# Kernel tuning notes

Hardware: AMD Instinct MI355X
Metric: run time of the kernel (lower is better)

## Reference

```python
import jax, jax.numpy as jnp
import numpy as np

N_VERBS = 500
N_ROLES = 190
VOCAB = 2000
R = 6            # max_role_count
EMB = 512        # embed_hidden == lstm_hidden
MLP = 1024       # mlp_hidden
C = 512          # conv base size
H = W = 7
NP = H * W
NC = C + 2       # conv channels + 2 coord channels


def _lin(k, fan_in, fan_out):
    kw, kb = jax.random.split(k)
    s = 1.0 / np.sqrt(fan_in)
    return (jax.random.uniform(kw, (fan_in, fan_out), jnp.float32, -s, s),
            jax.random.uniform(kb, (fan_out,), jnp.float32, -s, s))


def setup_inputs() -> dict:
    key = jax.random.key(0)
    ks = jax.random.split(key, 16)
    inp = {}
    inp['conv_feat'] = jax.random.normal(ks[0], (2, C, H, W), jnp.float32)
    inp['verbs'] = jax.random.randint(ks[1], (2,), 0, N_VERBS, jnp.int32)
    inp['roles'] = jax.random.randint(ks[2], (2, R), 0, N_ROLES, jnp.int32)
    inp['verb_emb'] = jax.random.normal(ks[3], (N_VERBS, EMB), jnp.float32)
    inp['role_emb'] = jax.random.normal(ks[4], (N_ROLES + 1, EMB), jnp.float32)
    inp['vW1'], inp['vb1'] = _lin(ks[5], NP * C, MLP)
    inp['vW2'], inp['vb2'] = _lin(ks[6], MLP, MLP)
    inp['vW3'], inp['vb3'] = _lin(ks[7], MLP, N_VERBS)
    inp['gW1'], inp['gb1'] = _lin(ks[8], 2 * NC + EMB, MLP)
    inp['gW2'], inp['gb2'] = _lin(ks[9], MLP, MLP)
    inp['gW3'], inp['gb3'] = _lin(ks[10], MLP, 2 * MLP)
    inp['gW4'], inp['gb4'] = _lin(ks[11], 2 * MLP, 4 * MLP)
    inp['fW1'], inp['fb1'] = _lin(ks[12], 4 * MLP, 4 * MLP)
    inp['fW2'], inp['fb2'] = _lin(ks[13], 4 * MLP, 2 * MLP)
    inp['fW3'], inp['fb3'] = _lin(ks[14], 2 * MLP, VOCAB)
    return inp


def _coords():
    c = jnp.linspace(-4.0, 4.0, H)
    x = jnp.broadcast_to(c[None, :], (H, W))   # x varies along width
    y = jnp.broadcast_to(c[:, None], (H, W))   # y varies along height
    return jnp.stack([x, y]).reshape(2, NP).T  # [NP, 2]


def reference(conv_feat, verbs, roles, verb_emb, role_emb,
              vW1, vb1, vW2, vb2, vW3, vb3,
              gW1, gb1, gW2, gb2, gW3, gb3, gW4, gb4,
              fW1, fb1, fW2, fb2, fW3, fb3):
    relu = jax.nn.relu
    B = conv_feat.shape[0]

    # verb head
    flat = conv_feat.reshape(B, NP * C)
    v = relu(flat @ vW1 + vb1)
    v = relu(v @ vW2 + vb2)
    verb_pred = v @ vW3 + vb3                                  # [B, N_VERBS]

    # role-verb query
    rv = (verb_emb[verbs][:, None, :] * role_emb[roles]).reshape(B * R, EMB)

    # per-role conv features + coord channels -> [Bu, NP, NC]
    feat = jnp.broadcast_to(conv_feat[:, None], (B, R, C, H, W)).reshape(B * R, C, NP)
    feat = jnp.concatenate([feat.transpose(0, 2, 1),
                            jnp.broadcast_to(_coords()[None], (B * R, NP, 2))], axis=2)

    # first g layer: concat([o_j, o_i, qst]) @ gW1 == split matmuls + broadcast add
    Wa, Wb, Wc = gW1[:NC], gW1[NC:2 * NC], gW1[2 * NC:]
    A = feat @ Wa          # pairs with conv1 (index j)
    Bm = feat @ Wb         # pairs with conv2 (index i)
    Q = rv @ Wc
    h = relu(A[:, None, :, :] + Bm[:, :, None, :] + Q[:, None, None, :] + gb1)  # [Bu, NP, NP, MLP]
    h = relu(h @ gW2 + gb2)
    h = relu(h @ gW3 + gb3)
    h = relu(h @ gW4 + gb4)                                    # [Bu, NP, NP, 4*MLP]
    g = h.sum(axis=(1, 2))                                     # [Bu, 4*MLP]

    f = relu(g @ fW1 + fb1)
    f = relu(f @ fW2 + fb2)
    f = f @ fW3 + fb3                                          # [Bu, VOCAB]
    role_predict = f.reshape(B, R, VOCAB)
    return verb_pred, role_predict
```

## Files before the change

### kernel.cpp

```cpp
#include <hip/hip_runtime.h>
#include <cstdint>

typedef _Float16 f16;
typedef f16 f16x8 __attribute__((ext_vector_type(8)));
typedef f16 f16x4 __attribute__((ext_vector_type(4)));
typedef float f32x4 __attribute__((ext_vector_type(4)));

#define GROUP_ROWS 2560
#define VALID_ROWS 2401
#define TPG 10
#define NGROUP 12

template <bool B> struct BoolC { static constexpr bool value = B; };

__device__ __forceinline__ void gll16(const void* g, void* l) {
  __builtin_amdgcn_global_load_lds((const __attribute__((address_space(1))) void*)g,
                                   (__attribute__((address_space(3))) void*)l, 16, 0, 0);
}

__global__ void wtrans_all(const float* __restrict__ gW2, const float* __restrict__ gW3,
                           const float* __restrict__ gW4, f16* __restrict__ W2t,
                           f16* __restrict__ W3t, f16* __restrict__ W4t) {
  __shared__ float t[32][33];
  int blk = blockIdx.x;
  const float* W; f16* Wt; int K, N, local;
  if (blk < 1024)      { W = gW2; Wt = W2t; K = 1024; N = 1024; local = blk; }
  else if (blk < 3072) { W = gW3; Wt = W3t; K = 1024; N = 2048; local = blk - 1024; }
  else                 { W = gW4; Wt = W4t; K = 2048; N = 4096; local = blk - 3072; }
  int ntn = N >> 5;
  int k0 = (local / ntn) * 32, n0 = (local % ntn) * 32;
  int tx = threadIdx.x & 31, ty = threadIdx.x >> 5;
#pragma unroll
  for (int j = 0; j < 4; ++j)
    t[ty + j * 8][tx] = W[(size_t)(k0 + ty + j * 8) * N + n0 + tx];
  __syncthreads();
#pragma unroll
  for (int j = 0; j < 4; ++j)
    Wt[(size_t)(n0 + ty + j * 8) * K + k0 + tx] = (f16)t[tx][ty + j * 8];
}

__global__ void build_rv(const float* __restrict__ verb_emb, const float* __restrict__ role_emb,
                         const int* __restrict__ verbs, const int* __restrict__ roles,
                         float* __restrict__ rv) {
  int g = blockIdx.x;
  int b = g / 6;
  int v = verbs[b], ro = roles[g];
  for (int e = threadIdx.x; e < 512; e += 256)
    rv[g * 512 + e] = verb_emb[(size_t)v * 512 + e] * role_emb[(size_t)ro * 512 + e];
}

__global__ void build_AB_part(const float* __restrict__ conv, const float* __restrict__ gW1,
                              float* __restrict__ part) {
  int blk = blockIdx.x;
  int nq = blk & 3, bp = blk >> 2;
  int p = bp % 49, b = bp / 49;
  int n = nq * 256 + threadIdx.x;
  int ky = blockIdx.y;
  int k0 = ky * 66, k1 = k0 + 66;
  if (k1 > 514) k1 = 514;
  float accA = 0.f, accB = 0.f;
  for (int k = k0; k < k1; ++k) {
    float s;
    if (k < 512) s = conv[((size_t)b * 512 + k) * 49 + p];
    else {
      int c7 = (k == 512) ? (p % 7) : (p / 7);
      s = (float)(c7 - 3) * (4.0f / 3.0f);
    }
    accA = fmaf(s, gW1[(size_t)k * 1024 + n], accA);
    accB = fmaf(s, gW1[(size_t)(514 + k) * 1024 + n], accB);
  }
  size_t base = ((size_t)ky * 98 + bp) * 2048;
  part[base + n] = accA;
  part[base + 1024 + n] = accB;
}

__global__ void build_AB_fin(const float* __restrict__ part, float* __restrict__ A,
                             float* __restrict__ Bm) {
  int idx = blockIdx.x * 256 + threadIdx.x;
  if (idx >= 98 * 2048) return;
  int bp = idx >> 11, rem = idx & 2047;
  float s = 0.f;
#pragma unroll
  for (int ky = 0; ky < 8; ++ky) s += part[((size_t)ky * 98 + bp) * 2048 + rem];
  if (rem < 1024) A[(size_t)bp * 1024 + rem] = s;
  else Bm[(size_t)bp * 1024 + (rem - 1024)] = s;
}

__global__ void build_h1(const float* __restrict__ A, const float* __restrict__ Bm,
                         const float* __restrict__ Q, const float* __restrict__ gb1,
                         f16* __restrict__ h1, int g0) {
  int rc = blockIdx.x;
  int gl = rc / GROUP_ROWS;
  int li = rc % GROUP_ROWS;
  int g = g0 + gl;
  int b = g / 6;
  int kk = threadIdx.x * 4;
  f16x4* dst = (f16x4*)(h1 + (size_t)rc * 1024 + kk);
  if (li >= VALID_ROWS) {
    f16x4 z = {(f16)0.f, (f16)0.f, (f16)0.f, (f16)0.f};
    *dst = z;
    return;
  }
  int i = li / 49, j = li % 49;
  const float4 a = *(const float4*)(A + ((size_t)b * 49 + j) * 1024 + kk);
  const float4 bb = *(const float4*)(Bm + ((size_t)b * 49 + i) * 1024 + kk);
  const float4 q = *(const float4*)(Q + (size_t)g * 1024 + kk);
  const float4 bi = *(const float4*)(gb1 + kk);
  float v0 = a.x + bb.x + q.x + bi.x;
  float v1 = a.y + bb.y + q.y + bi.y;
  float v2 = a.z + bb.z + q.z + bi.z;
  float v3 = a.w + bb.w + q.w + bi.w;
  f16x4 r;
  r.x = (f16)(v0 > 0.f ? v0 : 0.f);
  r.y = (f16)(v1 > 0.f ? v1 : 0.f);
  r.z = (f16)(v2 > 0.f ? v2 : 0.f);
  r.w = (f16)(v3 > 0.f ? v3 : 0.f);
  *dst = r;
}

#define WV4 asm volatile("s_waitcnt vmcnt(4)" ::: "memory")
#define WV0 asm volatile("s_waitcnt vmcnt(0)" ::: "memory")

#define LDSA(buf, mf, cc) (*(const f16x8*)(ldsc + (buf)*32768 + arow + (mf)*2048 + (cc)*16))
#define LDSB(buf, nf, cc) (*(const f16x8*)(ldsc + 65536 + (buf)*32768 + brow + (nf)*2048 + (cc)*16))

#define LOADB(BF, buf) { \
  BF[0][0] = LDSB(buf, 0, c0); BF[0][1] = LDSB(buf, 0, c1); \
  BF[1][0] = LDSB(buf, 1, c0); BF[1][1] = LDSB(buf, 1, c1); \
  BF[2][0] = LDSB(buf, 2, c0); BF[2][1] = LDSB(buf, 2, c1); \
  BF[3][0] = LDSB(buf, 3, c0); BF[3][1] = LDSB(buf, 3, c1); }

#define STAGE_A(t, h) { \
  const f16* _g = Aglo + (long)(h) * (128L * K) + (long)(t) * 64; \
  char* _l = ldsc + ((t)&1)*32768 + ((h)*128 + wave*16)*128; \
  gll16(_g, _l); gll16(_g + 8L*K, _l + 1024); }

#define STAGE_B(t, h) { \
  const f16* _g = Bglo + (long)(h) * (128L * K) + (long)(t) * 64; \
  char* _l = ldsc + 65536 + ((t)&1)*32768 + ((h)*128 + wave*16)*128; \
  gll16(_g, _l); gll16(_g + 8L*K, _l + 1024); }

#define PHASE(q, buf, BF, STG, WT, POST) { \
  f16x8 a00 = LDSA(buf, 2*(q), c0);   f16x8 a01 = LDSA(buf, 2*(q), c1); \
  f16x8 a10 = LDSA(buf, 2*(q)+1, c0); f16x8 a11 = LDSA(buf, 2*(q)+1, c1); \
  STG; \
  WT; \
  __builtin_amdgcn_s_barrier(); \
  __builtin_amdgcn_s_setprio(1); \
  _Pragma("unroll") \
  for (int nf = 0; nf < 4; ++nf) { \
    acc[2*(q)][nf]   = __builtin_amdgcn_mfma_f32_16x16x32_f16(a00, BF[nf][0], acc[2*(q)][nf], 0, 0, 0); \
    acc[2*(q)][nf]   = __builtin_amdgcn_mfma_f32_16x16x32_f16(a01, BF[nf][1], acc[2*(q)][nf], 0, 0, 0); \
    acc[2*(q)+1][nf] = __builtin_amdgcn_mfma_f32_16x16x32_f16(a10, BF[nf][0], acc[2*(q)+1][nf], 0, 0, 0); \
    acc[2*(q)+1][nf] = __builtin_amdgcn_mfma_f32_16x16x32_f16(a11, BF[nf][1], acc[2*(q)+1][nf], 0, 0, 0); \
  } \
  __builtin_amdgcn_s_setprio(0); \
  POST; \
  __builtin_amdgcn_s_barrier(); \
}

template <int FUSED>
__global__ __launch_bounds__(512, 2)
void gemm256(const f16* __restrict__ A, const f16* __restrict__ Bt,
             const float* __restrict__ bias, f16* __restrict__ C,
             float* __restrict__ P, int N, int K, int ntiles, int mtile_off) {
  __shared__ __align__(16) char ldsbuf[131072];
  char* ldsc = ldsbuf;
  const int tid = threadIdx.x;
  const int wave = tid >> 6, lane = tid & 63;
  const int wm = wave >> 2, wn = wave & 3;
  const int lr = lane & 15, lk = lane >> 4;
  const int c0 = lk ^ (lr & 7), c1 = c0 ^ 4;
  const int arow = (wm * 128 + lr) * 128;
  const int brow = (wn * 64 + lr) * 128;

  int nwg = gridDim.x, id = blockIdx.x;
  int qq = nwg >> 3, rr8 = nwg & 7;
  int xcd = id & 7, idx = id >> 3;
  int wg = (xcd < rr8 ? xcd * (qq + 1) : rr8 * (qq + 1) + (xcd - rr8) * qq) + idx;
  const int mtile = wg / ntiles, ntile = wg % ntiles;
  const long m0 = (long)mtile * 256, n0 = (long)ntile * 256;

  const int srow = lane >> 3;
  const int schunk = (lane & 7) ^ srow;
  const f16* Aglo = A + (m0 + wave * 16 + srow) * (long)K + schunk * 8;
  const f16* Bglo = Bt + (n0 + wave * 16 + srow) * (long)K + schunk * 8;

  f32x4 acc[8][4] = {};
  f16x8 bFa[4][2], bFb[4][2];

  const int NI = K >> 7;

  STAGE_B(0, 0); STAGE_B(0, 1);
  STAGE_A(0, 0); STAGE_A(0, 1);
  STAGE_B(1, 0); STAGE_B(1, 1);
  WV4;
  __builtin_amdgcn_s_barrier();
  LOADB(bFa, 0);

  auto run_iter = [&](int i, auto lastTag) {
    constexpr bool LAST = decltype(lastTag)::value;
    PHASE(0, 0, bFa, STAGE_A(2*i+1, 0), ;, ;);
    PHASE(1, 0, bFa, STAGE_A(2*i+1, 1), ;, ;);
    PHASE(2, 0, bFa, if constexpr (!LAST) STAGE_B(2*i+2, 0), ;, ;);
    PHASE(3, 0, bFa, if constexpr (!LAST) STAGE_B(2*i+2, 1),
                 if constexpr (LAST) { WV0; } else { WV4; },
                 LOADB(bFb, 1));
    PHASE(0, 1, bFb, if constexpr (!LAST) STAGE_A(2*i+2, 0), ;, ;);
    PHASE(1, 1, bFb, if constexpr (!LAST) STAGE_A(2*i+2, 1), ;, ;);
    PHASE(2, 1, bFb, if constexpr (!LAST) STAGE_B(2*i+3, 0), ;, ;);
    PHASE(3, 1, bFb, if constexpr (!LAST) STAGE_B(2*i+3, 1),
                 if constexpr (!LAST) { WV4; },
                 if constexpr (!LAST) LOADB(bFa, 0));
  };
#pragma unroll 1
  for (int i = 0; i < NI - 1; ++i) run_iter(i, BoolC<false>{});
  run_iter(NI - 1, BoolC<true>{});

  if (FUSED == 0) {
    __syncthreads();
    f16* lt = (f16*)ldsc;
#pragma unroll
    for (int mf = 0; mf < 8; ++mf) {
#pragma unroll
      for (int nf = 0; nf < 4; ++nf) {
        const int col = wn * 64 + nf * 16 + lr;
        const float bv = bias[n0 + col];
#pragma unroll
        for (int r = 0; r < 4; ++r) {
          const int row = wm * 128 + mf * 16 + lk * 4 + r;
          float v = acc[mf][nf][r] + bv;
          v = v > 0.f ? v : 0.f;
          lt[row * 256 + (col ^ (((row >> 2) & 3) << 4))] = (f16)v;
        }
      }
    }
    __syncthreads();
    const int r0 = tid >> 5, ch = tid & 31;
#pragma unroll
    for (int p = 0; p < 16; ++p) {
      const int row = p * 16 + r0;
      const int chs = ch ^ (((row >> 2) & 3) << 1);
      f16x8 v = *(const f16x8*)(lt + row * 256 + chs * 8);
      *(f16x8*)(C + (m0 + row) * N + n0 + ch * 8) = v;
    }
  } else {
    float* csum = (float*)ldsc;
    const int mrel = (mtile % TPG) * 256 + wm * 128;
#pragma unroll
    for (int nf = 0; nf < 4; ++nf) {
      const int col = (int)n0 + wn * 64 + nf * 16 + lr;
      const float bv = bias[col];
      float s = 0.f;
#pragma unroll
      for (int mf = 0; mf < 8; ++mf) {
        const int rb = mrel + mf * 16 + lk * 4;
#pragma unroll
        for (int r = 0; r < 4; ++r) {
          float v = acc[mf][nf][r] + bv;
          v = v > 0.f ? v : 0.f;
          if (rb + r < VALID_ROWS) s += v;
        }
      }
      s += __shfl_xor(s, 16);
      s += __shfl_xor(s, 32);
      if (lk == 0) csum[wm * 256 + wn * 64 + nf * 16 + lr] = s;
    }
    __syncthreads();
    for (int t = tid; t < 256; t += 512)
      P[(long)(mtile_off + mtile) * N + n0 + t] = csum[t] + csum[256 + t];
  }
}

__global__ void reduce_g(const float* __restrict__ P, float* __restrict__ g) {
  int idx = blockIdx.x * 256 + threadIdx.x;
  if (idx >= NGROUP * 4096) return;
  int gi = idx >> 12, n = idx & 4095;
  float s = 0.f;
#pragma unroll
  for (int t = 0; t < TPG; ++t) s += P[(size_t)(gi * TPG + t) * 4096 + n];
  g[idx] = s;
}

template <int M>
__global__ void skinny_part(const float* __restrict__ X, const float* __restrict__ W,
                            float* __restrict__ P, int K, int N, int kchunk) {
  int n = blockIdx.x * 256 + threadIdx.x;
  int k0 = blockIdx.y * kchunk;
  int k1 = k0 + kchunk;
  if (k1 > K) k1 = K;
  if (n >= N) return;
  float acc[M];
#pragma unroll
  for (int m = 0; m < M; ++m) acc[m] = 0.f;
#pragma unroll 4
  for (int k = k0; k < k1; ++k) {
    float w = W[(size_t)k * N + n];
#pragma unroll
    for (int m = 0; m < M; ++m) acc[m] = fmaf(X[(size_t)m * K + k], w, acc[m]);
  }
#pragma unroll
  for (int m = 0; m < M; ++m) P[((size_t)blockIdx.y * M + m) * N + n] = acc[m];
}

template <int RELU>
__global__ void skinny_fin(const float* __restrict__ P, const float* __restrict__ bias,
                           float* __restrict__ dst, int M, int N, int KC) {
  int idx = blockIdx.x * 256 + threadIdx.x;
  if (idx >= M * N) return;
  int m = idx / N, n = idx - m * N;
  float s = bias ? bias[n] : 0.f;
  for (int kc = 0; kc < KC; ++kc) s += P[((size_t)kc * M + m) * N + n];
  if (RELU) s = s > 0.f ? s : 0.f;
  dst[idx] = s;
}

static inline void skinny(const float* X, const float* W, const float* bias, float* dst,
                          float* sp, int Mrows, int K, int N, int relu, hipStream_t stream) {
  int nx = (N + 255) / 256;
  int KC = 1024 / nx;
  if (KC > 256) KC = 256;
  int kmax = K / 16;
  if (kmax < 1) kmax = 1;
  if (KC > kmax) KC = kmax;
  int kchunk = (K + KC - 1) / KC;
  dim3 g1(nx, KC);
  if (Mrows == 2)
    skinny_part<2><<<g1, 256, 0, stream>>>(X, W, sp, K, N, kchunk);
  else
    skinny_part<12><<<g1, 256, 0, stream>>>(X, W, sp, K, N, kchunk);
  int blocks = (Mrows * N + 255) / 256;
  if (relu)
    skinny_fin<1><<<blocks, 256, 0, stream>>>(sp, bias, dst, Mrows, N, KC);
  else
    skinny_fin<0><<<blocks, 256, 0, stream>>>(sp, bias, dst, Mrows, N, KC);
}

extern "C" void kernel_launch(void* const* d_in, const int* in_sizes, int n_in,
                              void* d_out, int out_size, void* d_ws, size_t ws_size,
                              hipStream_t stream) {
  const float* conv = (const float*)d_in[0];
  const int* verbs = (const int*)d_in[1];
  const int* roles = (const int*)d_in[2];
  const float* verb_emb = (const float*)d_in[3];
  const float* role_emb = (const float*)d_in[4];
  const float* vW1 = (const float*)d_in[5];
  const float* vb1 = (const float*)d_in[6];
  const float* vW2 = (const float*)d_in[7];
  const float* vb2 = (const float*)d_in[8];
  const float* vW3 = (const float*)d_in[9];
  const float* vb3 = (const float*)d_in[10];
  const float* gW1 = (const float*)d_in[11];
  const float* gb1 = (const float*)d_in[12];
  const float* gW2 = (const float*)d_in[13];
  const float* gb2 = (const float*)d_in[14];
  const float* gW3 = (const float*)d_in[15];
  const float* gb3 = (const float*)d_in[16];
  const float* gW4 = (const float*)d_in[17];
  const float* gb4 = (const float*)d_in[18];
  const float* fW1 = (const float*)d_in[19];
  const float* fb1 = (const float*)d_in[20];
  const float* fW2 = (const float*)d_in[21];
  const float* fb2 = (const float*)d_in[22];
  const float* fW3 = (const float*)d_in[23];
  const float* fb3 = (const float*)d_in[24];
  float* out = (float*)d_out;

  char* w = (char*)d_ws;
  auto alloc = [&](size_t bytes) {
    char* p = w;
    w += (bytes + 255) & ~(size_t)255;
    return p;
  };
  f16* W2t = (f16*)alloc((size_t)1024 * 1024 * 2);
  f16* W3t = (f16*)alloc((size_t)2048 * 1024 * 2);
  f16* W4t = (f16*)alloc((size_t)4096 * 2048 * 2);
  float* P4 = (float*)alloc((size_t)NGROUP * TPG * 4096 * 4);
  float* Abuf = (float*)alloc((size_t)2 * 49 * 1024 * 4);
  float* Bbuf = (float*)alloc((size_t)2 * 49 * 1024 * 4);
  float* Qbuf = (float*)alloc((size_t)12 * 1024 * 4);
  float* rvb = (float*)alloc((size_t)12 * 512 * 4);
  float* gbuf = (float*)alloc((size_t)12 * 4096 * 4);
  float* sp = (float*)alloc((size_t)64 * 12 * 4096 * 4);
  float* f1b = (float*)alloc((size_t)12 * 4096 * 4);
  float* f2b = (float*)alloc((size_t)12 * 2048 * 4);
  float* v1b = (float*)alloc((size_t)2 * 1024 * 4);
  float* v2b = (float*)alloc((size_t)2 * 1024 * 4);

  size_t used = (size_t)(w - (char*)d_ws);
  size_t remain = ws_size > used ? ws_size - used : 0;
  static const int opts[6] = {12, 6, 4, 3, 2, 1};
  int gpc = 1;
  for (int i = 0; i < 6; ++i) {
    size_t need = (size_t)opts[i] * GROUP_ROWS * 4096 * 2 + 4096;
    if (need <= remain) { gpc = opts[i]; break; }
  }
  f16* h1 = (f16*)alloc((size_t)gpc * GROUP_ROWS * 1024 * 2);
  f16* h2 = (f16*)alloc((size_t)gpc * GROUP_ROWS * 1024 * 2);
  f16* h3 = (f16*)alloc((size_t)gpc * GROUP_ROWS * 2048 * 2);
  int nchunks = NGROUP / gpc;

  wtrans_all<<<1024 + 2048 + 8192, 256, 0, stream>>>(gW2, gW3, gW4, W2t, W3t, W4t);

  build_rv<<<12, 256, 0, stream>>>(verb_emb, role_emb, verbs, roles, rvb);
  build_AB_part<<<dim3(98 * 4, 8), 256, 0, stream>>>(conv, gW1, sp);
  build_AB_fin<<<(98 * 2048 + 255) / 256, 256, 0, stream>>>(sp, Abuf, Bbuf);
  skinny(rvb, gW1 + (size_t)1028 * 1024, nullptr, Qbuf, sp, 12, 512, 1024, 0, stream);

  skinny(conv, vW1, vb1, v1b, sp, 2, 25088, 1024, 1, stream);
  skinny(v1b, vW2, vb2, v2b, sp, 2, 1024, 1024, 1, stream);
  skinny(v2b, vW3, vb3, out, sp, 2, 1024, 500, 0, stream);

  for (int c = 0; c < nchunks; ++c) {
    int g0 = c * gpc;
    int Mc = gpc * GROUP_ROWS;
    int mt = Mc / 256;
    build_h1<<<Mc, 256, 0, stream>>>(Abuf, Bbuf, Qbuf, gb1, h1, g0);
    gemm256<0><<<4 * mt, 512, 0, stream>>>(h1, W2t, gb2, h2, nullptr, 1024, 1024, 4, 0);
    gemm256<0><<<8 * mt, 512, 0, stream>>>(h2, W3t, gb3, h3, nullptr, 2048, 1024, 8, 0);
    gemm256<1><<<16 * mt, 512, 0, stream>>>(h3, W4t, gb4, nullptr, P4, 4096, 2048, 16, g0 * TPG);
  }
  reduce_g<<<(NGROUP * 4096 + 255) / 256, 256, 0, stream>>>(P4, gbuf);

  skinny(gbuf, fW1, fb1, f1b, sp, 12, 4096, 4096, 1, stream);
  skinny(f1b, fW2, fb2, f2b, sp, 12, 4096, 2048, 1, stream);
  skinny(f2b, fW3, fb3, out + 1000, sp, 12, 2048, 2000, 0, stream);

  (void)in_sizes; (void)n_in; (void)out_size; (void)ws_size;
}
```

Before: 934.5 us.

## Fuse h1 construction into first g-layer GEMM A-operand staging

Removes the separate build_h1 kernel and its f16 h1 buffer. The first GEMM (FUSED==2) now builds each A tile on the fly from A, Bm, Q and gb1 with fp32 loads, add, relu and an f16 convert, writing straight to LDS. This saves the h1 write and re-read and one launch. In exchange, the staging goes from async global_load_lds to synchronous register loads plus VALU work inside the MFMA pipeline, which needs extra lgkmcnt waits and may stall the main loop.

```diff
diff --git a/kernel.cpp b/kernel.cpp
--- a/kernel.cpp
+++ b/kernel.cpp
@@ -86,40 +86,9 @@
   else Bm[(size_t)bp * 1024 + (rem - 1024)] = s;
 }
 
-__global__ void build_h1(const float* __restrict__ A, const float* __restrict__ Bm,
-                         const float* __restrict__ Q, const float* __restrict__ gb1,
-                         f16* __restrict__ h1, int g0) {
-  int rc = blockIdx.x;
-  int gl = rc / GROUP_ROWS;
-  int li = rc % GROUP_ROWS;
-  int g = g0 + gl;
-  int b = g / 6;
-  int kk = threadIdx.x * 4;
-  f16x4* dst = (f16x4*)(h1 + (size_t)rc * 1024 + kk);
-  if (li >= VALID_ROWS) {
-    f16x4 z = {(f16)0.f, (f16)0.f, (f16)0.f, (f16)0.f};
-    *dst = z;
-    return;
-  }
-  int i = li / 49, j = li % 49;
-  const float4 a = *(const float4*)(A + ((size_t)b * 49 + j) * 1024 + kk);
-  const float4 bb = *(const float4*)(Bm + ((size_t)b * 49 + i) * 1024 + kk);
-  const float4 q = *(const float4*)(Q + (size_t)g * 1024 + kk);
-  const float4 bi = *(const float4*)(gb1 + kk);
-  float v0 = a.x + bb.x + q.x + bi.x;
-  float v1 = a.y + bb.y + q.y + bi.y;
-  float v2 = a.z + bb.z + q.z + bi.z;
-  float v3 = a.w + bb.w + q.w + bi.w;
-  f16x4 r;
-  r.x = (f16)(v0 > 0.f ? v0 : 0.f);
-  r.y = (f16)(v1 > 0.f ? v1 : 0.f);
-  r.z = (f16)(v2 > 0.f ? v2 : 0.f);
-  r.w = (f16)(v3 > 0.f ? v3 : 0.f);
-  *dst = r;
-}
-
 #define WV4 asm volatile("s_waitcnt vmcnt(4)" ::: "memory")
 #define WV0 asm volatile("s_waitcnt vmcnt(0)" ::: "memory")
+#define LGF { if constexpr (FUSED == 2) { asm volatile("s_waitcnt lgkmcnt(0)" ::: "memory"); } }
 
 #define LDSA(buf, mf, cc) (*(const f16x8*)(ldsc + (buf)*32768 + arow + (mf)*2048 + (cc)*16))
 #define LDSB(buf, nf, cc) (*(const f16x8*)(ldsc + 65536 + (buf)*32768 + brow + (nf)*2048 + (cc)*16))
@@ -139,6 +108,37 @@
   const f16* _g = Bglo + (long)(h) * (128L * K) + (long)(t) * 64; \
   char* _l = ldsc + 65536 + ((t)&1)*32768 + ((h)*128 + wave*16)*128; \
   gll16(_g, _l); gll16(_g + 8L*K, _l + 1024); }
+
+#define STAGE_H1(t, h) { \
+  const int _k0 = (t) * 64 + schunk * 8; \
+  const float4 _g0 = *(const float4*)(gbv + _k0); \
+  const float4 _g1 = *(const float4*)(gbv + _k0 + 4); \
+  char* _dst = ldsc + ((t)&1)*32768 + ((h)*128 + wave*16)*128 + lane*16; \
+  _Pragma("unroll") \
+  for (int _rr = 0; _rr < 2; ++_rr) { \
+    const float* _pa = rowA[(h)*2+_rr]; \
+    const float* _pb = rowB[(h)*2+_rr]; \
+    const float* _pq = rowQ[(h)*2+_rr]; \
+    f16x8 _w; \
+    if (_pa) { \
+      float4 _a0 = *(const float4*)(_pa + _k0), _a1 = *(const float4*)(_pa + _k0 + 4); \
+      float4 _b0 = *(const float4*)(_pb + _k0), _b1 = *(const float4*)(_pb + _k0 + 4); \
+      float4 _q0 = *(const float4*)(_pq + _k0), _q1 = *(const float4*)(_pq + _k0 + 4); \
+      float _v0 = _a0.x + _b0.x + _q0.x + _g0.x, _v1 = _a0.y + _b0.y + _q0.y + _g0.y; \
+      float _v2 = _a0.z + _b0.z + _q0.z + _g0.z, _v3 = _a0.w + _b0.w + _q0.w + _g0.w; \
+      float _v4 = _a1.x + _b1.x + _q1.x + _g1.x, _v5 = _a1.y + _b1.y + _q1.y + _g1.y; \
+      float _v6 = _a1.z + _b1.z + _q1.z + _g1.z, _v7 = _a1.w + _b1.w + _q1.w + _g1.w; \
+      _w[0] = (f16)(_v0 > 0.f ? _v0 : 0.f); _w[1] = (f16)(_v1 > 0.f ? _v1 : 0.f); \
+      _w[2] = (f16)(_v2 > 0.f ? _v2 : 0.f); _w[3] = (f16)(_v3 > 0.f ? _v3 : 0.f); \
+      _w[4] = (f16)(_v4 > 0.f ? _v4 : 0.f); _w[5] = (f16)(_v5 > 0.f ? _v5 : 0.f); \
+      _w[6] = (f16)(_v6 > 0.f ? _v6 : 0.f); _w[7] = (f16)(_v7 > 0.f ? _v7 : 0.f); \
+    } else { \
+      _Pragma("unroll") for (int _e = 0; _e < 8; ++_e) _w[_e] = (f16)0.f; \
+    } \
+    *(f16x8*)(_dst + _rr*1024) = _w; \
+  } }
+
+#define STG_A(t, h) { if constexpr (FUSED == 2) { STAGE_H1(t, h); } else { STAGE_A(t, h); } }
 
 #define PHASE(q, buf, BF, STG, WT, POST) { \
   f16x8 a00 = LDSA(buf, 2*(q), c0);   f16x8 a01 = LDSA(buf, 2*(q), c1); \
@@ -163,7 +163,10 @@
 __global__ __launch_bounds__(512, 2)
 void gemm256(const f16* __restrict__ A, const f16* __restrict__ Bt,
              const float* __restrict__ bias, f16* __restrict__ C,
-             float* __restrict__ P, int N, int K, int ntiles, int mtile_off) {
+             float* __restrict__ P,
+             const float* __restrict__ Ab, const float* __restrict__ Bb,
+             const float* __restrict__ Qb, const float* __restrict__ gbv,
+             int N, int K, int ntiles, int aux) {
   __shared__ __align__(16) char ldsbuf[131072];
   char* ldsc = ldsbuf;
   const int tid = threadIdx.x;
@@ -183,8 +186,30 @@
 
   const int srow = lane >> 3;
   const int schunk = (lane & 7) ^ srow;
-  const f16* Aglo = A + (m0 + wave * 16 + srow) * (long)K + schunk * 8;
+  const f16* Aglo = ((FUSED == 2) ? Bt : A) + (m0 + wave * 16 + srow) * (long)K + schunk * 8;
   const f16* Bglo = Bt + (n0 + wave * 16 + srow) * (long)K + schunk * 8;
+
+  const float* rowA[4];
+  const float* rowB[4];
+  const float* rowQ[4];
+  if constexpr (FUSED == 2) {
+#pragma unroll
+    for (int r = 0; r < 4; ++r) {
+      int h = r >> 1, rr = r & 1;
+      long mrow = (long)aux * GROUP_ROWS + m0 + h * 128 + wave * 16 + srow + rr * 8;
+      int g = (int)(mrow / GROUP_ROWS);
+      int li = (int)(mrow % GROUP_ROWS);
+      if (li < VALID_ROWS) {
+        int b = g / 6;
+        int ii = li / 49, jj = li % 49;
+        rowA[r] = Ab + ((size_t)b * 49 + jj) * 1024;
+        rowB[r] = Bb + ((size_t)b * 49 + ii) * 1024;
+        rowQ[r] = Qb + (size_t)g * 1024;
+      } else {
+        rowA[r] = nullptr; rowB[r] = nullptr; rowQ[r] = nullptr;
+      }
+    }
+  }
 
   f32x4 acc[8][4] = {};
   f16x8 bFa[4][2], bFb[4][2];
@@ -192,32 +217,33 @@
   const int NI = K >> 7;
 
   STAGE_B(0, 0); STAGE_B(0, 1);
-  STAGE_A(0, 0); STAGE_A(0, 1);
+  STG_A(0, 0); STG_A(0, 1);
   STAGE_B(1, 0); STAGE_B(1, 1);
   WV4;
+  LGF;
   __builtin_amdgcn_s_barrier();
   LOADB(bFa, 0);
 
   auto run_iter = [&](int i, auto lastTag) {
     constexpr bool LAST = decltype(lastTag)::value;
-    PHASE(0, 0, bFa, STAGE_A(2*i+1, 0), ;, ;);
-    PHASE(1, 0, bFa, STAGE_A(2*i+1, 1), ;, ;);
+    PHASE(0, 0, bFa, STG_A(2*i+1, 0), ;, ;);
+    PHASE(1, 0, bFa, STG_A(2*i+1, 1), ;, ;);
     PHASE(2, 0, bFa, if constexpr (!LAST) STAGE_B(2*i+2, 0), ;, ;);
     PHASE(3, 0, bFa, if constexpr (!LAST) STAGE_B(2*i+2, 1),
-                 if constexpr (LAST) { WV0; } else { WV4; },
+                 { if constexpr (LAST) { WV0; } else { WV4; } LGF; },
                  LOADB(bFb, 1));
-    PHASE(0, 1, bFb, if constexpr (!LAST) STAGE_A(2*i+2, 0), ;, ;);
-    PHASE(1, 1, bFb, if constexpr (!LAST) STAGE_A(2*i+2, 1), ;, ;);
+    PHASE(0, 1, bFb, if constexpr (!LAST) STG_A(2*i+2, 0), ;, ;);
+    PHASE(1, 1, bFb, if constexpr (!LAST) STG_A(2*i+2, 1), ;, ;);
     PHASE(2, 1, bFb, if constexpr (!LAST) STAGE_B(2*i+3, 0), ;, ;);
     PHASE(3, 1, bFb, if constexpr (!LAST) STAGE_B(2*i+3, 1),
-                 if constexpr (!LAST) { WV4; },
+                 { if constexpr (!LAST) { WV4; } LGF; },
                  if constexpr (!LAST) LOADB(bFa, 0));
   };
 #pragma unroll 1
   for (int i = 0; i < NI - 1; ++i) run_iter(i, BoolC<false>{});
   run_iter(NI - 1, BoolC<true>{});
 
-  if (FUSED == 0) {
+  if constexpr (FUSED != 1) {
     __syncthreads();
     f16* lt = (f16*)ldsc;
 #pragma unroll
@@ -268,7 +294,7 @@
     }
     __syncthreads();
     for (int t = tid; t < 256; t += 512)
-      P[(long)(mtile_off + mtile) * N + n0 + t] = csum[t] + csum[256 + t];
+      P[(long)(aux + mtile) * N + n0 + t] = csum[t] + csum[256 + t];
   }
 }
 
@@ -392,10 +418,9 @@
   static const int opts[6] = {12, 6, 4, 3, 2, 1};
   int gpc = 1;
   for (int i = 0; i < 6; ++i) {
-    size_t need = (size_t)opts[i] * GROUP_ROWS * 4096 * 2 + 4096;
+    size_t need = (size_t)opts[i] * GROUP_ROWS * 3072 * 2 + 4096;
     if (need <= remain) { gpc = opts[i]; break; }
   }
-  f16* h1 = (f16*)alloc((size_t)gpc * GROUP_ROWS * 1024 * 2);
   f16* h2 = (f16*)alloc((size_t)gpc * GROUP_ROWS * 1024 * 2);
   f16* h3 = (f16*)alloc((size_t)gpc * GROUP_ROWS * 2048 * 2);
   int nchunks = NGROUP / gpc;
@@ -415,10 +440,12 @@
     int g0 = c * gpc;
     int Mc = gpc * GROUP_ROWS;
     int mt = Mc / 256;
-    build_h1<<<Mc, 256, 0, stream>>>(Abuf, Bbuf, Qbuf, gb1, h1, g0);
-    gemm256<0><<<4 * mt, 512, 0, stream>>>(h1, W2t, gb2, h2, nullptr, 1024, 1024, 4, 0);
-    gemm256<0><<<8 * mt, 512, 0, stream>>>(h2, W3t, gb3, h3, nullptr, 2048, 1024, 8, 0);
-    gemm256<1><<<16 * mt, 512, 0, stream>>>(h3, W4t, gb4, nullptr, P4, 4096, 2048, 16, g0 * TPG);
+    gemm256<2><<<4 * mt, 512, 0, stream>>>(nullptr, W2t, gb2, h2, nullptr,
+                                           Abuf, Bbuf, Qbuf, gb1, 1024, 1024, 4, g0);
+    gemm256<0><<<8 * mt, 512, 0, stream>>>(h2, W3t, gb3, h3, nullptr,
+                                           nullptr, nullptr, nullptr, nullptr, 2048, 1024, 8, 0);
+    gemm256<1><<<16 * mt, 512, 0, stream>>>(h3, W4t, gb4, nullptr, P4,
+                                            nullptr, nullptr, nullptr, nullptr, 4096, 2048, 16, g0 * TPG);
   }
   reduce_g<<<(NGROUP * 4096 + 255) / 256, 256, 0, stream>>>(P4, gbuf);
 
```

After: 1.110 ms. 18.8% more time.

## Merge prep kernels into one launch and ride verb-head layers on GEMM grids

Applied to the files above, without the earlier changes.

Several small setup kernels are folded into one block-indexed kernel: weight transpose, A/B projection partials, the Q projection (now computed directly from the embeddings) and the vW1 split-K partials. A second kernel does the finish reductions. The verb head's second and third layers now run as extra side blocks appended to the first chunk's gemm256 launches. The goal is to cut launch count and serial tail latency by overlapping tiny, latency-bound work with big kernels. The cost is extra branching in the GEMM kernel, and the side blocks may hold 512-thread slots with large LDS while doing slow scalar dot products.

```diff
diff --git a/kernel.cpp b/kernel.cpp
--- a/kernel.cpp
+++ b/kernel.cpp
@@ -18,72 +18,107 @@
                                    (__attribute__((address_space(3))) void*)l, 16, 0, 0);
 }
 
-__global__ void wtrans_all(const float* __restrict__ gW2, const float* __restrict__ gW3,
-                           const float* __restrict__ gW4, f16* __restrict__ W2t,
-                           f16* __restrict__ W3t, f16* __restrict__ W4t) {
+__global__ void prep1(const float* __restrict__ gW2, const float* __restrict__ gW3,
+                      const float* __restrict__ gW4, f16* __restrict__ W2t,
+                      f16* __restrict__ W3t, f16* __restrict__ W4t,
+                      const float* __restrict__ conv, const float* __restrict__ gW1,
+                      float* __restrict__ abP,
+                      const float* __restrict__ verb_emb, const float* __restrict__ role_emb,
+                      const int* __restrict__ verbs, const int* __restrict__ roles,
+                      float* __restrict__ Qbuf,
+                      const float* __restrict__ vW1, float* __restrict__ vp) {
   __shared__ float t[32][33];
-  int blk = blockIdx.x;
-  const float* W; f16* Wt; int K, N, local;
-  if (blk < 1024)      { W = gW2; Wt = W2t; K = 1024; N = 1024; local = blk; }
-  else if (blk < 3072) { W = gW3; Wt = W3t; K = 1024; N = 2048; local = blk - 1024; }
-  else                 { W = gW4; Wt = W4t; K = 2048; N = 4096; local = blk - 3072; }
-  int ntn = N >> 5;
-  int k0 = (local / ntn) * 32, n0 = (local % ntn) * 32;
-  int tx = threadIdx.x & 31, ty = threadIdx.x >> 5;
-#pragma unroll
-  for (int j = 0; j < 4; ++j)
-    t[ty + j * 8][tx] = W[(size_t)(k0 + ty + j * 8) * N + n0 + tx];
-  __syncthreads();
-#pragma unroll
-  for (int j = 0; j < 4; ++j)
-    Wt[(size_t)(n0 + ty + j * 8) * K + k0 + tx] = (f16)t[tx][ty + j * 8];
-}
-
-__global__ void build_rv(const float* __restrict__ verb_emb, const float* __restrict__ role_emb,
-                         const int* __restrict__ verbs, const int* __restrict__ roles,
-                         float* __restrict__ rv) {
-  int g = blockIdx.x;
-  int b = g / 6;
-  int v = verbs[b], ro = roles[g];
-  for (int e = threadIdx.x; e < 512; e += 256)
-    rv[g * 512 + e] = verb_emb[(size_t)v * 512 + e] * role_emb[(size_t)ro * 512 + e];
-}
-
-__global__ void build_AB_part(const float* __restrict__ conv, const float* __restrict__ gW1,
-                              float* __restrict__ part) {
-  int blk = blockIdx.x;
-  int nq = blk & 3, bp = blk >> 2;
-  int p = bp % 49, b = bp / 49;
-  int n = nq * 256 + threadIdx.x;
-  int ky = blockIdx.y;
-  int k0 = ky * 66, k1 = k0 + 66;
-  if (k1 > 514) k1 = 514;
-  float accA = 0.f, accB = 0.f;
-  for (int k = k0; k < k1; ++k) {
-    float s;
-    if (k < 512) s = conv[((size_t)b * 512 + k) * 49 + p];
-    else {
-      int c7 = (k == 512) ? (p % 7) : (p / 7);
-      s = (float)(c7 - 3) * (4.0f / 3.0f);
-    }
-    accA = fmaf(s, gW1[(size_t)k * 1024 + n], accA);
-    accB = fmaf(s, gW1[(size_t)(514 + k) * 1024 + n], accB);
-  }
-  size_t base = ((size_t)ky * 98 + bp) * 2048;
-  part[base + n] = accA;
-  part[base + 1024 + n] = accB;
-}
-
-__global__ void build_AB_fin(const float* __restrict__ part, float* __restrict__ A,
-                             float* __restrict__ Bm) {
-  int idx = blockIdx.x * 256 + threadIdx.x;
-  if (idx >= 98 * 2048) return;
-  int bp = idx >> 11, rem = idx & 2047;
-  float s = 0.f;
-#pragma unroll
-  for (int ky = 0; ky < 8; ++ky) s += part[((size_t)ky * 98 + bp) * 2048 + rem];
-  if (rem < 1024) A[(size_t)bp * 1024 + rem] = s;
-  else Bm[(size_t)bp * 1024 + (rem - 1024)] = s;
+  int id = blockIdx.x;
+  if (id < 11264) {
+    const float* W; f16* Wt; int K, N, local;
+    if (id < 1024)      { W = gW2; Wt = W2t; K = 1024; N = 1024; local = id; }
+    else if (id < 3072) { W = gW3; Wt = W3t; K = 1024; N = 2048; local = id - 1024; }
+    else                { W = gW4; Wt = W4t; K = 2048; N = 4096; local = id - 3072; }
+    int ntn = N >> 5;
+    int k0 = (local / ntn) * 32, n0 = (local % ntn) * 32;
+    int tx = threadIdx.x & 31, ty = threadIdx.x >> 5;
+#pragma unroll
+    for (int j = 0; j < 4; ++j)
+      t[ty + j * 8][tx] = W[(size_t)(k0 + ty + j * 8) * N + n0 + tx];
+    __syncthreads();
+#pragma unroll
+    for (int j = 0; j < 4; ++j)
+      Wt[(size_t)(n0 + ty + j * 8) * K + k0 + tx] = (f16)t[tx][ty + j * 8];
+  } else if (id < 14400) {
+    int local = id - 11264;
+    int ky = local / 392, blk = local % 392;
+    int nq = blk & 3, bp = blk >> 2;
+    int p = bp % 49, b = bp / 49;
+    int n = nq * 256 + threadIdx.x;
+    int k0 = ky * 66, k1 = k0 + 66;
+    if (k1 > 514) k1 = 514;
+    float accA = 0.f, accB = 0.f;
+    for (int k = k0; k < k1; ++k) {
+      float s;
+      if (k < 512) s = conv[((size_t)b * 512 + k) * 49 + p];
+      else {
+        int c7 = (k == 512) ? (p % 7) : (p / 7);
+        s = (float)(c7 - 3) * (4.0f / 3.0f);
+      }
+      accA = fmaf(s, gW1[(size_t)k * 1024 + n], accA);
+      accB = fmaf(s, gW1[(size_t)(514 + k) * 1024 + n], accB);
+    }
+    size_t base = ((size_t)ky * 98 + bp) * 2048;
+    abP[base + n] = accA;
+    abP[base + 1024 + n] = accB;
+  } else if (id < 14448) {
+    int local = id - 14400;
+    int g = local >> 2, nq = local & 3;
+    int b = g / 6;
+    int v = verbs[b], ro = roles[g];
+    int n = nq * 256 + threadIdx.x;
+    const float* ve = verb_emb + (size_t)v * 512;
+    const float* re = role_emb + (size_t)ro * 512;
+    const float* Wc = gW1 + (size_t)1028 * 1024;
+    float acc = 0.f;
+#pragma unroll 4
+    for (int e = 0; e < 512; ++e)
+      acc = fmaf(ve[e] * re[e], Wc[(size_t)e * 1024 + n], acc);
+    Qbuf[(size_t)g * 1024 + n] = acc;
+  } else {
+    int local = id - 14448;
+    int nblk = local & 3, kc = local >> 2;
+    int n = nblk * 256 + threadIdx.x;
+    int k0 = kc * 392, k1 = k0 + 392;
+    if (k1 > 25088) k1 = 25088;
+    float a0 = 0.f, a1 = 0.f;
+#pragma unroll 4
+    for (int k = k0; k < k1; ++k) {
+      float w = vW1[(size_t)k * 1024 + n];
+      a0 = fmaf(conv[k], w, a0);
+      a1 = fmaf(conv[25088 + k], w, a1);
+    }
+    vp[((size_t)kc * 2 + 0) * 1024 + n] = a0;
+    vp[((size_t)kc * 2 + 1) * 1024 + n] = a1;
+  }
+}
+
+__global__ void prep2(const float* __restrict__ abP, float* __restrict__ A,
+                      float* __restrict__ Bm, const float* __restrict__ vp,
+                      const float* __restrict__ vb1, float* __restrict__ v1b) {
+  int id = blockIdx.x;
+  if (id < 784) {
+    int idx = id * 256 + threadIdx.x;
+    if (idx >= 98 * 2048) return;
+    int bp = idx >> 11, rem = idx & 2047;
+    float s = 0.f;
+#pragma unroll
+    for (int ky = 0; ky < 8; ++ky) s += abP[((size_t)ky * 98 + bp) * 2048 + rem];
+    if (rem < 1024) A[(size_t)bp * 1024 + rem] = s;
+    else Bm[(size_t)bp * 1024 + (rem - 1024)] = s;
+  } else {
+    int idx = (id - 784) * 256 + threadIdx.x;
+    int m = idx >> 10, n = idx & 1023;
+    float s = vb1[n];
+#pragma unroll 4
+    for (int kc = 0; kc < 64; ++kc) s += vp[((size_t)kc * 2 + m) * 1024 + n];
+    v1b[idx] = s > 0.f ? s : 0.f;
+  }
 }
 
 __global__ void build_h1(const float* __restrict__ A, const float* __restrict__ Bm,
@@ -163,10 +198,37 @@
 __global__ __launch_bounds__(512, 2)
 void gemm256(const f16* __restrict__ A, const f16* __restrict__ Bt,
              const float* __restrict__ bias, f16* __restrict__ C,
-             float* __restrict__ P, int N, int K, int ntiles, int mtile_off) {
+             float* __restrict__ P,
+             const float* __restrict__ sx, const float* __restrict__ sw,
+             const float* __restrict__ sbias, float* __restrict__ so,
+             int sideKind, int gemmN, int N, int K, int ntiles, int aux) {
   __shared__ __align__(16) char ldsbuf[131072];
   char* ldsc = ldsbuf;
   const int tid = threadIdx.x;
+
+  if ((int)blockIdx.x >= gemmN) {
+    int sb = blockIdx.x - gemmN;
+    int idx = sb * 512 + tid;
+    if (sideKind == 2) {
+      int m = idx >> 10, n = idx & 1023;
+      float s = sbias[n];
+#pragma unroll 8
+      for (int k = 0; k < 1024; ++k)
+        s = fmaf(sx[(size_t)m * 1024 + k], sw[(size_t)k * 1024 + n], s);
+      so[idx] = s > 0.f ? s : 0.f;
+    } else if (sideKind == 3) {
+      if (idx < 1000) {
+        int m = idx / 500, n = idx % 500;
+        float s = sbias[n];
+#pragma unroll 8
+        for (int k = 0; k < 1024; ++k)
+          s = fmaf(sx[(size_t)m * 1024 + k], sw[(size_t)k * 500 + n], s);
+        so[idx] = s;
+      }
+    }
+    return;
+  }
+
   const int wave = tid >> 6, lane = tid & 63;
   const int wm = wave >> 2, wn = wave & 3;
   const int lr = lane & 15, lk = lane >> 4;
@@ -174,7 +236,7 @@
   const int arow = (wm * 128 + lr) * 128;
   const int brow = (wn * 64 + lr) * 128;
 
-  int nwg = gridDim.x, id = blockIdx.x;
+  int nwg = gemmN, id = blockIdx.x;
   int qq = nwg >> 3, rr8 = nwg & 7;
   int xcd = id & 7, idx = id >> 3;
   int wg = (xcd < rr8 ? xcd * (qq + 1) : rr8 * (qq + 1) + (xcd - rr8) * qq) + idx;
@@ -268,7 +330,7 @@
     }
     __syncthreads();
     for (int t = tid; t < 256; t += 512)
-      P[(long)(mtile_off + mtile) * N + n0 + t] = csum[t] + csum[256 + t];
+      P[(long)(aux + mtile) * N + n0 + t] = csum[t] + csum[256 + t];
   }
 }
 
@@ -282,7 +344,6 @@
   g[idx] = s;
 }
 
-template <int M>
 __global__ void skinny_part(const float* __restrict__ X, const float* __restrict__ W,
                             float* __restrict__ P, int K, int N, int kchunk) {
   int n = blockIdx.x * 256 + threadIdx.x;
@@ -290,33 +351,33 @@
   int k1 = k0 + kchunk;
   if (k1 > K) k1 = K;
   if (n >= N) return;
-  float acc[M];
-#pragma unroll
-  for (int m = 0; m < M; ++m) acc[m] = 0.f;
+  float acc[12];
+#pragma unroll
+  for (int m = 0; m < 12; ++m) acc[m] = 0.f;
 #pragma unroll 4
   for (int k = k0; k < k1; ++k) {
     float w = W[(size_t)k * N + n];
 #pragma unroll
-    for (int m = 0; m < M; ++m) acc[m] = fmaf(X[(size_t)m * K + k], w, acc[m]);
-  }
-#pragma unroll
-  for (int m = 0; m < M; ++m) P[((size_t)blockIdx.y * M + m) * N + n] = acc[m];
+    for (int m = 0; m < 12; ++m) acc[m] = fmaf(X[(size_t)m * K + k], w, acc[m]);
+  }
+#pragma unroll
+  for (int m = 0; m < 12; ++m) P[((size_t)blockIdx.y * 12 + m) * N + n] = acc[m];
 }
 
 template <int RELU>
 __global__ void skinny_fin(const float* __restrict__ P, const float* __restrict__ bias,
-                           float* __restrict__ dst, int M, int N, int KC) {
+                           float* __restrict__ dst, int N, int KC) {
   int idx = blockIdx.x * 256 + threadIdx.x;
-  if (idx >= M * N) return;
+  if (idx >= 12 * N) return;
   int m = idx / N, n = idx - m * N;
   float s = bias ? bias[n] : 0.f;
-  for (int kc = 0; kc < KC; ++kc) s += P[((size_t)kc * M + m) * N + n];
+  for (int kc = 0; kc < KC; ++kc) s += P[((size_t)kc * 12 + m) * N + n];
   if (RELU) s = s > 0.f ? s : 0.f;
   dst[idx] = s;
 }
 
 static inline void skinny(const float* X, const float* W, const float* bias, float* dst,
-                          float* sp, int Mrows, int K, int N, int relu, hipStream_t stream) {
+                          float* sp, int K, int N, int relu, hipStream_t stream) {
   int nx = (N + 255) / 256;
   int KC = 1024 / nx;
   if (KC > 256) KC = 256;
@@ -325,15 +386,12 @@
   if (KC > kmax) KC = kmax;
   int kchunk = (K + KC - 1) / KC;
   dim3 g1(nx, KC);
-  if (Mrows == 2)
-    skinny_part<2><<<g1, 256, 0, stream>>>(X, W, sp, K, N, kchunk);
+  skinny_part<<<g1, 256, 0, stream>>>(X, W, sp, K, N, kchunk);
+  int blocks = (12 * N + 255) / 256;
+  if (relu)
+    skinny_fin<1><<<blocks, 256, 0, stream>>>(sp, bias, dst, N, KC);
   else
-    skinny_part<12><<<g1, 256, 0, stream>>>(X, W, sp, K, N, kchunk);
-  int blocks = (Mrows * N + 255) / 256;
-  if (relu)
-    skinny_fin<1><<<blocks, 256, 0, stream>>>(sp, bias, dst, Mrows, N, KC);
-  else
-    skinny_fin<0><<<blocks, 256, 0, stream>>>(sp, bias, dst, Mrows, N, KC);
+    skinny_fin<0><<<blocks, 256, 0, stream>>>(sp, bias, dst, N, KC);
 }
 
 extern "C" void kernel_launch(void* const* d_in, const int* in_sizes, int n_in,
@@ -379,9 +437,10 @@
   float* Abuf = (float*)alloc((size_t)2 * 49 * 1024 * 4);
   float* Bbuf = (float*)alloc((size_t)2 * 49 * 1024 * 4);
   float* Qbuf = (float*)alloc((size_t)12 * 1024 * 4);
-  float* rvb = (float*)alloc((size_t)12 * 512 * 4);
   float* gbuf = (float*)alloc((size_t)12 * 4096 * 4);
-  float* sp = (float*)alloc((size_t)64 * 12 * 4096 * 4);
+  float* sp = (float*)alloc((size_t)128 * 12 * 4096 * 4);
+  float* abP = (float*)alloc((size_t)8 * 98 * 2048 * 4);
+  float* vp = (float*)alloc((size_t)64 * 2 * 1024 * 4);
   float* f1b = (float*)alloc((size_t)12 * 4096 * 4);
   float* f2b = (float*)alloc((size_t)12 * 2048 * 4);
   float* v1b = (float*)alloc((size_t)2 * 1024 * 4);
@@ -400,31 +459,33 @@
   f16* h3 = (f16*)alloc((size_t)gpc * GROUP_ROWS * 2048 * 2);
   int nchunks = NGROUP / gpc;
 
-  wtrans_all<<<1024 + 2048 + 8192, 256, 0, stream>>>(gW2, gW3, gW4, W2t, W3t, W4t);
-
-  build_rv<<<12, 256, 0, stream>>>(verb_emb, role_emb, verbs, roles, rvb);
-  build_AB_part<<<dim3(98 * 4, 8), 256, 0, stream>>>(conv, gW1, sp);
-  build_AB_fin<<<(98 * 2048 + 255) / 256, 256, 0, stream>>>(sp, Abuf, Bbuf);
-  skinny(rvb, gW1 + (size_t)1028 * 1024, nullptr, Qbuf, sp, 12, 512, 1024, 0, stream);
-
-  skinny(conv, vW1, vb1, v1b, sp, 2, 25088, 1024, 1, stream);
-  skinny(v1b, vW2, vb2, v2b, sp, 2, 1024, 1024, 1, stream);
-  skinny(v2b, vW3, vb3, out, sp, 2, 1024, 500, 0, stream);
+  prep1<<<15472, 256, 0, stream>>>(gW2, gW3, gW4, W2t, W3t, W4t,
+                                   conv, gW1, abP,
+                                   verb_emb, role_emb, verbs, roles, Qbuf,
+                                   vW1, vp);
+  prep2<<<792, 256, 0, stream>>>(abP, Abuf, Bbuf, vp, vb1, v1b);
 
   for (int c = 0; c < nchunks; ++c) {
     int g0 = c * gpc;
     int Mc = gpc * GROUP_ROWS;
     int mt = Mc / 256;
+    int s2 = (c == 0) ? 4 : 0, s3 = (c == 0) ? 2 : 0;
     build_h1<<<Mc, 256, 0, stream>>>(Abuf, Bbuf, Qbuf, gb1, h1, g0);
-    gemm256<0><<<4 * mt, 512, 0, stream>>>(h1, W2t, gb2, h2, nullptr, 1024, 1024, 4, 0);
-    gemm256<0><<<8 * mt, 512, 0, stream>>>(h2, W3t, gb3, h3, nullptr, 2048, 1024, 8, 0);
-    gemm256<1><<<16 * mt, 512, 0, stream>>>(h3, W4t, gb4, nullptr, P4, 4096, 2048, 16, g0 * TPG);
+    gemm256<0><<<4 * mt + s2, 512, 0, stream>>>(h1, W2t, gb2, h2, nullptr,
+                                                v1b, vW2, vb2, v2b, 2, 4 * mt,
+                                                1024, 1024, 4, 0);
+    gemm256<0><<<8 * mt + s3, 512, 0, stream>>>(h2, W3t, gb3, h3, nullptr,
+                                                v2b, vW3, vb3, out, 3, 8 * mt,
+                                                2048, 1024, 8, 0);
+    gemm256<1><<<16 * mt, 512, 0, stream>>>(h3, W4t, gb4, nullptr, P4,
+                                            nullptr, nullptr, nullptr, nullptr, 0, 16 * mt,
+                                            4096, 2048, 16, g0 * TPG);
   }
   reduce_g<<<(NGROUP * 4096 + 255) / 256, 256, 0, stream>>>(P4, gbuf);
 
-  skinny(gbuf, fW1, fb1, f1b, sp, 12, 4096, 4096, 1, stream);
-  skinny(f1b, fW2, fb2, f2b, sp, 12, 4096, 2048, 1, stream);
-  skinny(f2b, fW3, fb3, out + 1000, sp, 12, 2048, 2000, 0, stream);
+  skinny(gbuf, fW1, fb1, f1b, sp, 4096, 4096, 1, stream);
+  skinny(f1b, fW2, fb2, f2b, sp, 4096, 2048, 1, stream);
+  skinny(f2b, fW3, fb3, out + 1000, sp, 2048, 2000, 0, stream);
 
   (void)in_sizes; (void)n_in; (void)out_size; (void)ws_size;
 }
```

Result: no change. 943.5 us (+1.0%).
